# Kernel optimization log

Hardware: AMD Instinct MI355X
Metric: run time of the kernel (lower is better)

The kernel has to match this reference:

```python
import jax, jax.numpy as jnp
import numpy as np

B, S, HID = 2, 2048, 2048
NH, NG = 32, 8
HD = HID // NH  # 64
KV = HD * NG    # 512


def setup_inputs() -> dict:
    key = jax.random.key(0)
    ks = jax.random.split(key, 9)
    w = lambda k, shp: jax.random.normal(k, shp, dtype=jnp.float32) * 0.02
    return {
        "hidden_state": jax.random.normal(ks[0], (B, S, HID), dtype=jnp.float32),
        "Wq": w(ks[1], (HID, HID)), "bq": jnp.zeros((HID,), jnp.float32),
        "Wk": w(ks[2], (HID, KV)),  "bk": jnp.zeros((KV,), jnp.float32),
        "Wv": w(ks[3], (HID, KV)),  "bv": jnp.zeros((KV,), jnp.float32),
        "Wo": w(ks[4], (HID, HID)), "bo": jnp.zeros((HID,), jnp.float32),
    }


def reference(hidden_state, Wq, bq, Wk, bk, Wv, bv, Wo, bo):
    bs, seq, _ = hidden_state.shape
    rep = NH // NG  # heads per KV group

    q = hidden_state @ Wq + bq                      # [B,S,HID]
    k = hidden_state @ Wk + bk                      # [B,S,KV]
    v = hidden_state @ Wv + bv

    q = q.reshape(bs, seq, NH, HD).transpose(0, 2, 1, 3)   # [B,NH,S,D]
    k = k.reshape(bs, seq, NG, HD).transpose(0, 2, 1, 3)   # [B,NG,S,D]
    v = v.reshape(bs, seq, NG, HD).transpose(0, 2, 1, 3)
    # grouped-KV expansion: each group repeated consecutively rep times
    k = jnp.repeat(k, rep, axis=1)                          # [B,NH,S,D]
    v = jnp.repeat(v, rep, axis=1)

    scores = jnp.einsum("bhqd,bhkd->bhqk", q, k) / jnp.sqrt(jnp.float32(HD))
    probs = jax.nn.softmax(scores, axis=-1)
    out = jnp.einsum("bhqk,bhkd->bhqd", probs, v)           # [B,NH,S,D]
    out = out.transpose(0, 2, 1, 3).reshape(bs, seq, HID)
    return out @ Wo + bo
```

## Files before the change

### kernel.cpp

```cpp
#include <hip/hip_runtime.h>
#include <hip/hip_bf16.h>
#include <math.h>

typedef __bf16 bf16x8 __attribute__((ext_vector_type(8)));
typedef float f32x4 __attribute__((ext_vector_type(4)));
typedef __hip_bfloat16 bf16_t;

#define MFMA_BF16(a, b, c) __builtin_amdgcn_mfma_f32_16x16x32_bf16((a), (b), (c), 0, 0, 0)

__device__ __forceinline__ void async_copy16(const bf16_t* g, bf16_t* lds_base) {
  __builtin_amdgcn_global_load_lds(
      (const __attribute__((address_space(1))) unsigned int*)g,
      (__attribute__((address_space(3))) unsigned int*)lds_base,
      16, 0, 0);
}

__device__ __forceinline__ unsigned fbits(float x) { return __builtin_bit_cast(unsigned, x); }

__global__ __launch_bounds__(256) void prep(
    const float* __restrict__ hidden, const float* __restrict__ Wq, const float* __restrict__ Wk,
    const float* __restrict__ Wv, const float* __restrict__ Wo,
    const float* __restrict__ bq, const float* __restrict__ bk, const float* __restrict__ bv,
    bf16_t* __restrict__ hiddenB, bf16_t* __restrict__ WqkvT, bf16_t* __restrict__ WoT,
    float* __restrict__ bqkv, float c1) {
  __shared__ float tile[64][65];
  int bid = blockIdx.x;
  const int t = threadIdx.x;
  if (bid < 8192) {
    const int i = bid * 256 + t;
    float4 v = ((const float4*)hidden)[i];
    union { bf16_t h[4]; ushort4 u; } cv;
    cv.h[0] = __float2bfloat16(v.x);
    cv.h[1] = __float2bfloat16(v.y);
    cv.h[2] = __float2bfloat16(v.z);
    cv.h[3] = __float2bfloat16(v.w);
    ((ushort4*)hiddenB)[i] = cv.u;
    return;
  }
  bid -= 8192;
  if (bid >= 2560) {
    const int i = (bid - 2560) * 256 + t;
    float v;
    if (i < 2048) v = bq[i] * c1;
    else if (i < 2560) v = bk[i - 2048];
    else v = bv[i - 2560];
    bqkv[i] = v;
    return;
  }
  const float* src;
  bf16_t* dst;
  int Cc, bx, by;
  float scale = 1.0f;
  if (bid < 1024) { src = Wq; dst = WqkvT; Cc = 2048; bx = bid & 31; by = bid >> 5; scale = c1; }
  else if (bid < 1280) { bid -= 1024; src = Wk; dst = WqkvT + (size_t)2048 * 2048; Cc = 512; bx = bid & 7; by = bid >> 3; }
  else if (bid < 1536) { bid -= 1280; src = Wv; dst = WqkvT + (size_t)2560 * 2048; Cc = 512; bx = bid & 7; by = bid >> 3; }
  else { bid -= 1536; src = Wo; dst = WoT; Cc = 2048; bx = bid & 31; by = bid >> 5; }
  const int tx = t & 63, ty = t >> 6;
  const int c0 = bx * 64, r0 = by * 64;
#pragma unroll
  for (int i = ty; i < 64; i += 4)
    tile[i][tx] = src[(size_t)(r0 + i) * Cc + c0 + tx];
  __syncthreads();
#pragma unroll
  for (int i = ty; i < 64; i += 4)
    dst[(size_t)(c0 + i) * 2048 + r0 + tx] = __float2bfloat16(tile[tx][i] * scale);
}

template <typename TOUT>
__global__ __launch_bounds__(256, 3) void gemm_bt(
    const bf16_t* __restrict__ A, const bf16_t* __restrict__ Bt,
    const float* __restrict__ bias, TOUT* __restrict__ C, bf16_t* __restrict__ vTp,
    int M, int N, int K) {
  __shared__ alignas(16) bf16_t As[128 * 64];
  __shared__ alignas(16) bf16_t Bs[128 * 64];

  const int tid = threadIdx.x;
  const int w = tid >> 6, lane = tid & 63;
  const int quad = lane >> 4, l16 = lane & 15;
  const int wm = w >> 1, wn = w & 1;
  const int m0 = blockIdx.y * 128, n0 = blockIdx.x * 128;

  f32x4 acc[4][4] = {};

  const int rr = lane >> 3;
  const int scol = ((lane & 7) ^ rr) * 8;
  const int sx = l16 & 7;

  for (int k0 = 0; k0 < K; k0 += 64) {
    __syncthreads();
#pragma unroll
    for (int c = 0; c < 4; ++c) {
      const int r = w * 32 + c * 8 + rr;
      async_copy16(A + (size_t)(m0 + r) * K + k0 + scol, &As[(w * 32 + c * 8) * 64]);
      async_copy16(Bt + (size_t)(n0 + r) * K + k0 + scol, &Bs[(w * 32 + c * 8) * 64]);
    }
    __syncthreads();

#pragma unroll
    for (int kh = 0; kh < 2; ++kh) {
      bf16x8 af[4], bf[4];
#pragma unroll
      for (int i = 0; i < 4; ++i) {
        af[i] = *(const bf16x8*)&As[(wm * 64 + i * 16 + l16) * 64 + (((kh * 4 + quad) ^ sx) * 8)];
        bf[i] = *(const bf16x8*)&Bs[(wn * 64 + i * 16 + l16) * 64 + (((kh * 4 + quad) ^ sx) * 8)];
      }
#pragma unroll
      for (int i = 0; i < 4; ++i)
#pragma unroll
        for (int j = 0; j < 4; ++j)
          acc[i][j] = MFMA_BF16(af[i], bf[j], acc[i][j]);
    }
  }

  if (vTp != nullptr && n0 >= 2560) {
#pragma unroll
    for (int i = 0; i < 4; ++i) {
      const int row = m0 + wm * 64 + i * 16 + quad * 4;
      const int bb = row >> 11, s = row & 2047;
#pragma unroll
      for (int j = 0; j < 4; ++j) {
        const int col = n0 + wn * 64 + j * 16 + l16;
        const float bv = bias[col];
        union { bf16_t h[4]; ushort4 u; } cv;
#pragma unroll
        for (int r = 0; r < 4; ++r) cv.h[r] = __float2bfloat16(acc[i][j][r] + bv);
        *(ushort4*)&vTp[((size_t)bb * 512 + (col - 2560)) * 2048 + s] = cv.u;
      }
    }
    return;
  }

#pragma unroll
  for (int i = 0; i < 4; ++i) {
    const int row = m0 + wm * 64 + i * 16 + quad * 4;
#pragma unroll
    for (int j = 0; j < 4; ++j) {
      const int col = n0 + wn * 64 + j * 16 + l16;
      const float bv = bias[col];
#pragma unroll
      for (int r = 0; r < 4; ++r) {
        const float val = acc[i][j][r] + bv;
        if constexpr (__is_same(TOUT, float)) {
          C[(size_t)(row + r) * N + col] = val;
        } else {
          C[(size_t)(row + r) * N + col] = __float2bfloat16(val);
        }
      }
    }
  }
}

__global__ __launch_bounds__(512, 2) void gemm256(
    const bf16_t* __restrict__ A, const bf16_t* __restrict__ Bt,
    const float* __restrict__ bias, bf16_t* __restrict__ C, bf16_t* __restrict__ vTp) {
  constexpr int N = 3072, K = 2048;
  __shared__ alignas(16) bf16_t As[2 * 256 * 64];
  __shared__ alignas(16) bf16_t Bs[2 * 256 * 64];

  const int tid = threadIdx.x;
  const int w = tid >> 6, lane = tid & 63;
  const int quad = lane >> 4, l16 = lane & 15;
  const int wm = w >> 2, wn = w & 3;

  const int flat = blockIdx.y * 12 + blockIdx.x;
  const int swz = (flat & 7) * 24 + (flat >> 3);
  const int m0 = (swz / 12) * 256, n0 = (swz % 12) * 256;

  const int rr = lane >> 3, c7 = lane & 7;
  const int scol = (c7 ^ rr) * 8;
  const int sx = l16 & 7;

  auto stA = [&](int t, int h) {
    const int kb = (t & 31) * 64;
    const int rbase = h * 128 + w * 8;
    bf16_t* d0 = &As[(t & 1) * (256 * 64) + rbase * 64];
    const bf16_t* s0 = A + (size_t)(m0 + rbase + rr) * K + kb + scol;
    async_copy16(s0, d0);
    async_copy16(s0 + (size_t)64 * K, d0 + 64 * 64);
  };
  auto stB = [&](int t, int h) {
    const int kb = (t & 31) * 64;
    const int rbase = h * 128 + w * 8;
    bf16_t* d0 = &Bs[(t & 1) * (256 * 64) + rbase * 64];
    const bf16_t* s0 = Bt + (size_t)(n0 + rbase + rr) * K + kb + scol;
    async_copy16(s0, d0);
    async_copy16(s0 + (size_t)64 * K, d0 + 64 * 64);
  };

  f32x4 acc[4][2][4] = {};

  stB(0, 0); stB(0, 1); stA(0, 0); stA(0, 1);
  stB(1, 0); stB(1, 1);
  asm volatile("s_waitcnt vmcnt(4)" ::: "memory");
  __builtin_amdgcn_s_barrier();
  __builtin_amdgcn_sched_barrier(0);

  for (int it = 0; it < 16; ++it) {
    const int kt = it * 2;
#pragma unroll
    for (int kg = 0; kg < 2; ++kg) {
      const int ta = (kt + kg + 1) & 31;
      const int tb = (kt + kg + 2) & 31;
      const bf16_t* Asb = &As[kg * (256 * 64)];
      const bf16_t* Bsb = &Bs[kg * (256 * 64)];
      bf16x8 b[4][2];
#pragma unroll
      for (int p = 0; p < 4; ++p) {
        if (p == 0) {
#pragma unroll
          for (int ni = 0; ni < 4; ++ni)
#pragma unroll
            for (int kk = 0; kk < 2; ++kk)
              b[ni][kk] = *(const bf16x8*)&Bsb[(wn * 64 + ni * 16 + l16) * 64 +
                                               (((kk * 4 + quad) ^ sx) * 8)];
        }
        bf16x8 a[2][2];
#pragma unroll
        for (int mi = 0; mi < 2; ++mi)
#pragma unroll
          for (int kk = 0; kk < 2; ++kk)
            a[mi][kk] = *(const bf16x8*)&Asb[(wm * 128 + p * 32 + mi * 16 + l16) * 64 +
                                             (((kk * 4 + quad) ^ sx) * 8)];
        if (p == 0) stA(ta, 0);
        else if (p == 1) stA(ta, 1);
        else if (p == 2) stB(tb, 0);
        else stB(tb, 1);
        __builtin_amdgcn_s_barrier();
        __builtin_amdgcn_s_setprio(1);
#pragma unroll
        for (int kk = 0; kk < 2; ++kk)
#pragma unroll
          for (int mi = 0; mi < 2; ++mi)
#pragma unroll
            for (int ni = 0; ni < 4; ++ni)
              acc[p][mi][ni] = MFMA_BF16(a[mi][kk], b[ni][kk], acc[p][mi][ni]);
        __builtin_amdgcn_s_setprio(0);
        if (p == 3) {
          asm volatile("s_waitcnt vmcnt(4)" ::: "memory");
          __builtin_amdgcn_s_barrier();
          __builtin_amdgcn_sched_barrier(0);
        } else {
          __builtin_amdgcn_s_barrier();
        }
      }
    }
  }

  asm volatile("s_waitcnt vmcnt(0)" ::: "memory");

  if (n0 >= 2560) {
#pragma unroll
    for (int p = 0; p < 4; ++p)
#pragma unroll
      for (int mi = 0; mi < 2; ++mi) {
        const int row4 = m0 + wm * 128 + p * 32 + mi * 16 + quad * 4;
        const int bb = row4 >> 11, s = row4 & 2047;
#pragma unroll
        for (int ni = 0; ni < 4; ++ni) {
          const int col = n0 + wn * 64 + ni * 16 + l16;
          const float bv = bias[col];
          union { bf16_t h[4]; ushort4 u; } cv;
#pragma unroll
          for (int r = 0; r < 4; ++r) cv.h[r] = __float2bfloat16(acc[p][mi][ni][r] + bv);
          *(ushort4*)&vTp[((size_t)bb * 512 + (col - 2560)) * 2048 + s] = cv.u;
        }
      }
    return;
  }

#pragma unroll
  for (int p = 0; p < 4; ++p)
#pragma unroll
    for (int mi = 0; mi < 2; ++mi) {
      const int row4 = m0 + wm * 128 + p * 32 + mi * 16 + quad * 4;
#pragma unroll
      for (int ni = 0; ni < 4; ++ni) {
        const int col = n0 + wn * 64 + ni * 16 + l16;
        const float bv = bias[col];
#pragma unroll
        for (int r = 0; r < 4; ++r)
          C[(size_t)(row4 + r) * N + col] = __float2bfloat16(acc[p][mi][ni][r] + bv);
      }
    }
}

__global__ __launch_bounds__(256, 4) void gqa_attn(
    const bf16_t* __restrict__ QKV, const bf16_t* __restrict__ VT, bf16_t* __restrict__ O,
    int xoff) {
  constexpr int S = 2048, HID = 2048, QKVS = 3072, HD = 64;
  const int tid = threadIdx.x;
  const int w = tid >> 6, lane = tid & 63;
  const int quad = lane >> 4, l16 = lane & 15;
  const int hp = blockIdx.y, b = blockIdx.z;
  const int h = hp * 2 + (w & 1);
  const int g = hp >> 1;
  const int q0 = (xoff + blockIdx.x) * 64 + (w >> 1) * 32;

  __shared__ alignas(16) bf16_t Ks[64 * 64];
  __shared__ alignas(16) bf16_t VTs[64 * 64];
  __shared__ alignas(16) bf16_t Ps[128 * 64];

  bf16x8 qf[2][2];
#pragma unroll
  for (int mt = 0; mt < 2; ++mt)
#pragma unroll
    for (int ks = 0; ks < 2; ++ks)
      qf[mt][ks] = *(const bf16x8*)&QKV[(size_t)(b * S + q0 + mt * 16 + l16) * QKVS +
                                        h * HD + ks * 32 + quad * 8];

  const int rr = lane >> 3, c7 = lane & 7;
  const int sx = l16 & 7;

  const bf16_t* Kbase = QKV + (size_t)b * S * QKVS + 2048 + g * HD;
  const bf16_t* Vbase = VT + (size_t)(b * 512 + g * HD) * S;

  const int srow = w * 16 + rr;
  const bf16_t* kp0 = Kbase + (size_t)srow * QKVS + c7 * 8;
  const bf16_t* kp1 = kp0 + (size_t)8 * QKVS;
  const bf16_t* vp0 = Vbase + (size_t)srow * S + c7 * 8;
  const bf16_t* vp1 = vp0 + (size_t)8 * S;
  bf16_t* KsW0 = &Ks[(srow)*64 + (c7 ^ rr) * 8];
  bf16_t* KsW1 = KsW0 + 8 * 64;
  bf16_t* VsW0 = &VTs[(srow)*64 + (c7 ^ rr) * 8];
  bf16_t* VsW1 = VsW0 + 8 * 64;

  f32x4 oacc[2][4] = {};
  f32x4 lacc[2] = {};
  bf16x8 ones;
#pragma unroll
  for (int j = 0; j < 8; ++j) ones[j] = (__bf16)1.0f;

  uint4 kr0 = *(const uint4*)kp0;
  uint4 kr1 = *(const uint4*)kp1;
  uint4 vr0 = *(const uint4*)vp0;
  uint4 vr1 = *(const uint4*)vp1;

  for (int s0 = 0; s0 < S; s0 += 64) {
    __syncthreads();
    *(uint4*)KsW0 = kr0;
    *(uint4*)KsW1 = kr1;
    *(uint4*)VsW0 = vr0;
    *(uint4*)VsW1 = vr1;
    const int sn = (s0 + 64) & (S - 1);
    kr0 = *(const uint4*)(kp0 + (size_t)sn * QKVS);
    kr1 = *(const uint4*)(kp1 + (size_t)sn * QKVS);
    vr0 = *(const uint4*)(vp0 + sn);
    vr1 = *(const uint4*)(vp1 + sn);
    __syncthreads();

    __builtin_amdgcn_s_setprio(1);
#pragma unroll
    for (int nt = 0; nt < 4; ++nt) {
      bf16x8 kf0 = *(const bf16x8*)&Ks[(nt * 16 + l16) * 64 + ((quad ^ sx) * 8)];
      bf16x8 kf1 = *(const bf16x8*)&Ks[(nt * 16 + l16) * 64 + (((4 + quad) ^ sx) * 8)];
#pragma unroll
      for (int mt = 0; mt < 2; ++mt) {
        f32x4 s = {};
        s = MFMA_BF16(kf0, qf[mt][0], s);
        s = MFMA_BF16(kf1, qf[mt][1], s);
        const float p0 = __builtin_amdgcn_exp2f(s[0]);
        const float p1 = __builtin_amdgcn_exp2f(s[1]);
        const float p2 = __builtin_amdgcn_exp2f(s[2]);
        const float p3 = __builtin_amdgcn_exp2f(s[3]);
        uint2 pk;
        pk.x = __builtin_amdgcn_perm(fbits(p1), fbits(p0), 0x07060302);
        pk.y = __builtin_amdgcn_perm(fbits(p3), fbits(p2), 0x07060302);
        *(uint2*)&Ps[(w * 32 + mt * 16 + l16) * 64 +
                     (((nt * 2 + (quad >> 1)) ^ sx) * 8) + (quad & 1) * 4] = pk;
      }
    }

#pragma unroll
    for (int kc = 0; kc < 2; ++kc) {
      bf16x8 pf[2];
#pragma unroll
      for (int mt = 0; mt < 2; ++mt) {
        pf[mt] = *(const bf16x8*)&Ps[(w * 32 + mt * 16 + l16) * 64 + (((kc * 4 + quad) ^ sx) * 8)];
        lacc[mt] = MFMA_BF16(pf[mt], ones, lacc[mt]);
      }
#pragma unroll
      for (int dt = 0; dt < 4; ++dt) {
        bf16x8 vf = *(const bf16x8*)&VTs[(dt * 16 + l16) * 64 + (((kc * 4 + quad) ^ sx) * 8)];
#pragma unroll
        for (int mt = 0; mt < 2; ++mt)
          oacc[mt][dt] = MFMA_BF16(pf[mt], vf, oacc[mt][dt]);
      }
    }
    __builtin_amdgcn_s_setprio(0);
  }

#pragma unroll
  for (int mt = 0; mt < 2; ++mt) {
    float linv[4];
#pragma unroll
    for (int r = 0; r < 4; ++r) linv[r] = 1.0f / lacc[mt][r];
#pragma unroll
    for (int dt = 0; dt < 4; ++dt)
#pragma unroll
      for (int r = 0; r < 4; ++r)
        O[(size_t)(b * S + q0 + mt * 16 + quad * 4 + r) * HID + h * HD + dt * 16 + l16] =
            __float2bfloat16(oacc[mt][dt][r] * linv[r]);
  }
}

extern "C" void kernel_launch(void* const* d_in, const int* in_sizes, int n_in,
                              void* d_out, int out_size, void* d_ws, size_t ws_size,
                              hipStream_t stream) {
  const float* hidden = (const float*)d_in[0];
  const float* Wq = (const float*)d_in[1];
  const float* bq = (const float*)d_in[2];
  const float* Wk = (const float*)d_in[3];
  const float* bk = (const float*)d_in[4];
  const float* Wv = (const float*)d_in[5];
  const float* bv = (const float*)d_in[6];
  const float* Wo = (const float*)d_in[7];
  const float* bo = (const float*)d_in[8];
  float* out = (float*)d_out;

  constexpr int B = 2, S = 2048, HID = 2048, KV = 512, QKVN = 3072;
  constexpr int M = B * S;
  const float c1 = 0.125f * 1.44269504089f;

  char* ws = (char*)d_ws;
  bf16_t* hiddenB = (bf16_t*)ws; ws += (size_t)M * HID * 2;
  bf16_t* WqkvT = (bf16_t*)ws;   ws += (size_t)QKVN * HID * 2;
  bf16_t* WoT = (bf16_t*)ws;     ws += (size_t)HID * HID * 2;
  bf16_t* qkv = (bf16_t*)ws;     ws += (size_t)M * QKVN * 2;
  bf16_t* vT = (bf16_t*)ws;      ws += (size_t)M * KV * 2;
  bf16_t* attn = (bf16_t*)ws;    ws += (size_t)M * HID * 2;
  float* bqkv = (float*)ws;      ws += QKVN * 4;

  prep<<<8192 + 2560 + 12, 256, 0, stream>>>(hidden, Wq, Wk, Wv, Wo, bq, bk, bv,
                                             hiddenB, WqkvT, WoT, bqkv, c1);

  gemm256<<<dim3(QKVN / 256, M / 256), 512, 0, stream>>>(hiddenB, WqkvT, bqkv, qkv, vT);

  gqa_attn<<<dim3(S / 128, 16, B), 256, 0, stream>>>(qkv, vT, attn, 0);
  gqa_attn<<<dim3(S / 128, 16, B), 256, 0, stream>>>(qkv, vT, attn, 16);

  gemm_bt<float><<<dim3(HID / 128, M / 128), 256, 0, stream>>>(
      attn, WoT, bo, out, (bf16_t*)nullptr, M, HID, HID);
}
```

Measured before the change: 312.8 us.

## Restructure QKV GEMM main loop into two phases and merge attention launches

```diff
diff --git a/kernel.cpp b/kernel.cpp
--- a/kernel.cpp
+++ b/kernel.cpp
@@ -196,53 +196,70 @@
   __builtin_amdgcn_sched_barrier(0);
 
   for (int it = 0; it < 16; ++it) {
-    const int kt = it * 2;
 #pragma unroll
     for (int kg = 0; kg < 2; ++kg) {
-      const int ta = (kt + kg + 1) & 31;
-      const int tb = (kt + kg + 2) & 31;
-      const bf16_t* Asb = &As[kg * (256 * 64)];
-      const bf16_t* Bsb = &Bs[kg * (256 * 64)];
+      const int t = it * 2 + kg;
+      const int ta = (t + 1) & 31;
+      const int tb = (t + 2) & 31;
+      const bf16_t* Asb = &As[(t & 1) * (256 * 64)];
+      const bf16_t* Bsb = &Bs[(t & 1) * (256 * 64)];
+
       bf16x8 b[4][2];
 #pragma unroll
-      for (int p = 0; p < 4; ++p) {
-        if (p == 0) {
-#pragma unroll
-          for (int ni = 0; ni < 4; ++ni)
-#pragma unroll
-            for (int kk = 0; kk < 2; ++kk)
-              b[ni][kk] = *(const bf16x8*)&Bsb[(wn * 64 + ni * 16 + l16) * 64 +
-                                               (((kk * 4 + quad) ^ sx) * 8)];
-        }
-        bf16x8 a[2][2];
+      for (int ni = 0; ni < 4; ++ni)
+#pragma unroll
+        for (int kk = 0; kk < 2; ++kk)
+          b[ni][kk] = *(const bf16x8*)&Bsb[(wn * 64 + ni * 16 + l16) * 64 +
+                                           (((kk * 4 + quad) ^ sx) * 8)];
+      bf16x8 a01[2][2][2];
+#pragma unroll
+      for (int p = 0; p < 2; ++p)
 #pragma unroll
         for (int mi = 0; mi < 2; ++mi)
 #pragma unroll
           for (int kk = 0; kk < 2; ++kk)
-            a[mi][kk] = *(const bf16x8*)&Asb[(wm * 128 + p * 32 + mi * 16 + l16) * 64 +
-                                             (((kk * 4 + quad) ^ sx) * 8)];
-        if (p == 0) stA(ta, 0);
-        else if (p == 1) stA(ta, 1);
-        else if (p == 2) stB(tb, 0);
-        else stB(tb, 1);
-        __builtin_amdgcn_s_barrier();
-        __builtin_amdgcn_s_setprio(1);
+            a01[p][mi][kk] = *(const bf16x8*)&Asb[(wm * 128 + p * 32 + mi * 16 + l16) * 64 +
+                                                  (((kk * 4 + quad) ^ sx) * 8)];
+      stA(ta, 0); stA(ta, 1);
+      __builtin_amdgcn_s_barrier();
+      __builtin_amdgcn_s_setprio(1);
+#pragma unroll
+      for (int p = 0; p < 2; ++p)
 #pragma unroll
         for (int kk = 0; kk < 2; ++kk)
 #pragma unroll
           for (int mi = 0; mi < 2; ++mi)
 #pragma unroll
             for (int ni = 0; ni < 4; ++ni)
-              acc[p][mi][ni] = MFMA_BF16(a[mi][kk], b[ni][kk], acc[p][mi][ni]);
-        __builtin_amdgcn_s_setprio(0);
-        if (p == 3) {
-          asm volatile("s_waitcnt vmcnt(4)" ::: "memory");
-          __builtin_amdgcn_s_barrier();
-          __builtin_amdgcn_sched_barrier(0);
-        } else {
-          __builtin_amdgcn_s_barrier();
-        }
-      }
+              acc[p][mi][ni] = MFMA_BF16(a01[p][mi][kk], b[ni][kk], acc[p][mi][ni]);
+      __builtin_amdgcn_s_setprio(0);
+      __builtin_amdgcn_s_barrier();
+
+      bf16x8 a23[2][2][2];
+#pragma unroll
+      for (int p = 0; p < 2; ++p)
+#pragma unroll
+        for (int mi = 0; mi < 2; ++mi)
+#pragma unroll
+          for (int kk = 0; kk < 2; ++kk)
+            a23[p][mi][kk] = *(const bf16x8*)&Asb[(wm * 128 + (p + 2) * 32 + mi * 16 + l16) * 64 +
+                                                  (((kk * 4 + quad) ^ sx) * 8)];
+      stB(tb, 0); stB(tb, 1);
+      __builtin_amdgcn_s_barrier();
+      __builtin_amdgcn_s_setprio(1);
+#pragma unroll
+      for (int p = 0; p < 2; ++p)
+#pragma unroll
+        for (int kk = 0; kk < 2; ++kk)
+#pragma unroll
+          for (int mi = 0; mi < 2; ++mi)
+#pragma unroll
+            for (int ni = 0; ni < 4; ++ni)
+              acc[p + 2][mi][ni] = MFMA_BF16(a23[p][mi][kk], b[ni][kk], acc[p + 2][mi][ni]);
+      __builtin_amdgcn_s_setprio(0);
+      asm volatile("s_waitcnt vmcnt(4)" ::: "memory");
+      __builtin_amdgcn_s_barrier();
+      __builtin_amdgcn_sched_barrier(0);
     }
   }
 
@@ -435,8 +452,7 @@
 
   gemm256<<<dim3(QKVN / 256, M / 256), 512, 0, stream>>>(hiddenB, WqkvT, bqkv, qkv, vT);
 
-  gqa_attn<<<dim3(S / 128, 16, B), 256, 0, stream>>>(qkv, vT, attn, 0);
-  gqa_attn<<<dim3(S / 128, 16, B), 256, 0, stream>>>(qkv, vT, attn, 16);
+  gqa_attn<<<dim3(S / 64, 16, B), 256, 0, stream>>>(qkv, vT, attn, 0);
 
   gemm_bt<float><<<dim3(HID / 128, M / 128), 256, 0, stream>>>(
       attn, WoT, bo, out, (bf16_t*)nullptr, M, HID, HID);
```

Result: no change. 311.2 us (-0.5%).
